# Kernel optimization log

Measured on AMD Instinct MI355X. Metric: run time of the kernel, lower is better.

The kernel has to match this reference:

```python
import jax, jax.numpy as jnp
import numpy as np

B, TQ, TP, H, A = 64, 64, 1024, 1024, 1024
NEG_INF = -1e30


def setup_inputs() -> dict:
    key = jax.random.key(0)
    ks = jax.random.split(key, 12)
    w = lambda k, shape, scale=0.02: (jax.random.normal(k, shape, jnp.float32) * scale)
    return dict(
        question=jax.random.normal(ks[0], (B, TQ, H), jnp.float32),
        question_mask=jnp.ones((B, TQ), jnp.float32),
        passage=jax.random.normal(ks[1], (B, TP, H), jnp.float32),
        passage_mask=jnp.ones((B, TP), jnp.float32),
        V_q=jax.random.normal(ks[2], (1, 1, H), jnp.float32),  # nn.Parameter(torch.randn)
        Wk_q=w(ks[3], (H, A)), Wq_q=w(ks[4], (H, A)), w_q=w(ks[5], (A,)),
        Wk_p=w(ks[6], (H, A)), Wq_p=w(ks[7], (H, A)), w_p=w(ks[8], (A,)),
        W_ih=w(ks[9], (3 * H, H)), W_hh=w(ks[10], (3 * H, H)),
        b_ih=jnp.zeros((3 * H,), jnp.float32), b_hh=jnp.zeros((3 * H,), jnp.float32),
    )


def _attn_pool(key_seq, query, mask, Wk, Wq, wv):
    """Additive attention pooling. key_seq: [T,B,H]; query: [1,B,Hq] or [1,1,Hq]
    (broadcasts over T and/or B); mask: [T,B]. Returns pooled [1,B,H], masked logits [T,B]."""
    s = jnp.tanh(key_seq @ Wk + query @ Wq) @ wv          # [T,B]
    s = jnp.where(mask > 0, s, NEG_INF)                    # mask invalid positions
    alpha = jax.nn.softmax(s, axis=0)                      # softmax over time
    pooled = jnp.einsum('tb,tbh->bh', alpha, key_seq)[None]
    return pooled, s


def _gru_cell(x, h, W_ih, W_hh, b_ih, b_hh):
    """torch.nn.GRUCell math. x, h: [B,H]."""
    gi = x @ W_ih.T + b_ih
    gh = h @ W_hh.T + b_hh
    i_r, i_z, i_n = jnp.split(gi, 3, axis=-1)
    h_r, h_z, h_n = jnp.split(gh, 3, axis=-1)
    r = jax.nn.sigmoid(i_r + h_r)
    z = jax.nn.sigmoid(i_z + h_z)
    n = jnp.tanh(i_n + r * h_n)
    return (1.0 - z) * n + z * h


def reference(question, question_mask, passage, passage_mask, V_q, Wk_q, Wq_q, w_q,
              Wk_p, Wq_p, w_p, W_ih, W_hh, b_ih, b_hh):
    # batch_first -> time-first
    q = jnp.transpose(question, (1, 0, 2))   # [TQ,B,H]
    qm = question_mask.T                     # [TQ,B]
    p = jnp.transpose(passage, (1, 0, 2))    # [TP,B,H]
    pm = passage_mask.T                      # [TP,B]
    # question pooling with learned query V_q (broadcast over T and B)
    hidden, _ = _attn_pool(q, V_q, qm, Wk_q, Wq_q, w_q)          # [1,B,H]
    # passage pooling with question summary as query -> start logits
    inputs, ans_begin = _attn_pool(p, hidden, pm, Wk_p, Wq_p, w_p)
    # one GRU decoding step (num_layers=1, no dropout/residual)
    out = _gru_cell(inputs[0], hidden[0], W_ih, W_hh, b_ih, b_hh)  # [B,H]
    # passage pooling with updated state -> end logits
    _, ans_end = _attn_pool(p, out[None], pm, Wk_p, Wq_p, w_p)
    return ans_begin.T, ans_end.T            # each [B,TP]
```

## Files before the change

kernel.cpp:

```cpp
#include <hip/hip_runtime.h>
#include <cstdint>
#include <cstddef>

typedef unsigned short u16;
typedef __bf16 bf16x8 __attribute__((ext_vector_type(8)));
typedef float floatx4 __attribute__((ext_vector_type(4)));

__device__ __forceinline__ u16 f32_to_bf16(float f) {
    unsigned u = __builtin_bit_cast(unsigned, f);
    u += 0x7fffu + ((u >> 16) & 1u);
    return (u16)(u >> 16);
}
__device__ __forceinline__ unsigned pack_bf16x2(float lo, float hi) {
    return (unsigned)f32_to_bf16(lo) | ((unsigned)f32_to_bf16(hi) << 16);
}
__device__ __forceinline__ float bf16_lo(unsigned u) {
    return __builtin_bit_cast(float, u << 16);
}
__device__ __forceinline__ float bf16_hi(unsigned u) {
    return __builtin_bit_cast(float, u & 0xffff0000u);
}
__device__ __forceinline__ float fast_tanh(float x) {
    float e = __expf(2.0f * x);
    return 1.0f - 2.0f * __builtin_amdgcn_rcpf(e + 1.0f);
}
__device__ __forceinline__ float fast_sigmoid(float x) {
    return __builtin_amdgcn_rcpf(1.0f + __expf(-x));
}
__device__ __forceinline__ void async_copy16(void* lds, const void* g) {
    __builtin_amdgcn_global_load_lds((const __attribute__((address_space(1))) void*)g,
                                     (__attribute__((address_space(3))) void*)lds,
                                     16, 0, 0);
}

__global__ __launch_bounds__(256) void conv_bf16_kernel(
    const float* __restrict__ in, u16* __restrict__ out)
{
    const size_t i = ((size_t)blockIdx.x * 256 + threadIdx.x) * 8;
    float4 a = *(const float4*)(in + i);
    float4 b = *(const float4*)(in + i + 4);
    uint4 o;
    o.x = pack_bf16x2(a.x, a.y);
    o.y = pack_bf16x2(a.z, a.w);
    o.z = pack_bf16x2(b.x, b.y);
    o.w = pack_bf16x2(b.z, b.w);
    *(uint4*)(out + i) = o;
}

__global__ __launch_bounds__(256) void transpose_bf16_kernel(
    const float* __restrict__ W, u16* __restrict__ WT, int K, int N)
{
    __shared__ float tile[32][33];
    const int k0 = blockIdx.y * 32, n0 = blockIdx.x * 32;
    const int tid = threadIdx.x;
#pragma unroll
    for (int i = 0; i < 4; ++i) {
        int e = tid + i * 256, rr = e >> 5, cc = e & 31;
        tile[rr][cc] = W[(size_t)(k0 + rr) * N + (n0 + cc)];
    }
    __syncthreads();
#pragma unroll
    for (int i = 0; i < 4; ++i) {
        int e = tid + i * 256, rr = e >> 5, cc = e & 31;
        WT[(size_t)(n0 + rr) * K + (k0 + cc)] = f32_to_bf16(tile[cc][rr]);
    }
}

__global__ __launch_bounds__(256) void vq_proj_kernel(
    const float* __restrict__ Vq, const float* __restrict__ Wq, float* __restrict__ out)
{
    const int a = blockIdx.x * 256 + threadIdx.x;
    const int h0 = blockIdx.y * 128;
    float acc = 0.f;
#pragma unroll 8
    for (int h = h0; h < h0 + 128; ++h)
        acc += Vq[h] * Wq[(size_t)h * 1024 + a];
    atomicAdd(&out[a], acc);
}

__global__ __launch_bounds__(256) void gemm_bf16_kernel(
    const u16* __restrict__ A, const u16* __restrict__ BT,
    u16* __restrict__ C, int M, int K, int N)
{
    __shared__ __align__(16) u16 As[128 * 32];
    __shared__ __align__(16) u16 Bs[128 * 32];
    const int tid  = threadIdx.x;
    const int lane = tid & 63;
    const int wave = tid >> 6;
    const int wm = (wave >> 1) * 64, wn = (wave & 1) * 64;
    const int quad = lane >> 4, lr = lane & 15;
    const int m0 = blockIdx.y * 128;
    const int n0 = blockIdx.x * 128;

    const int r0 = tid >> 2, c0 = (tid & 3) * 8;
    const u16* gA = A  + (size_t)(m0 + r0) * K + c0;
    const u16* gB = BT + (size_t)(n0 + r0) * K + c0;
    u16* lA0 = As + wave * 512;  u16* lA1 = lA0 + 2048;
    u16* lB0 = Bs + wave * 512;  u16* lB1 = lB0 + 2048;
    const size_t rowStride = (size_t)64 * K;

    floatx4 acc[4][4] = {};

    for (int k0 = 0; k0 < K; k0 += 32) {
        async_copy16(lA0, gA + k0);
        async_copy16(lA1, gA + rowStride + k0);
        async_copy16(lB0, gB + k0);
        async_copy16(lB1, gB + rowStride + k0);
        __syncthreads();
        bf16x8 af[4], bfr[4];
#pragma unroll
        for (int i = 0; i < 4; ++i)
            af[i] = *(const bf16x8*)(As + (wm + i * 16 + lr) * 32 + quad * 8);
#pragma unroll
        for (int j = 0; j < 4; ++j)
            bfr[j] = *(const bf16x8*)(Bs + (wn + j * 16 + lr) * 32 + quad * 8);
#pragma unroll
        for (int i = 0; i < 4; ++i)
#pragma unroll
            for (int j = 0; j < 4; ++j)
                acc[i][j] = __builtin_amdgcn_mfma_f32_16x16x32_bf16(af[i], bfr[j], acc[i][j], 0, 0, 0);
        __syncthreads();
    }
#pragma unroll
    for (int i = 0; i < 4; ++i) {
        int rb = m0 + wm + i * 16 + quad * 4;
#pragma unroll
        for (int j = 0; j < 4; ++j) {
            int col = n0 + wn + j * 16 + lr;
#pragma unroll
            for (int rg = 0; rg < 4; ++rg)
                C[(size_t)(rb + rg) * N + col] = f32_to_bf16(acc[i][j][rg]);
        }
    }
}

__global__ __launch_bounds__(256) void tanh_dot_kernel(
    const u16* __restrict__ R, const float* __restrict__ shift,
    const float* __restrict__ wv, const float* __restrict__ mask,
    float* __restrict__ out, int shiftDiv)
{
    const int row  = blockIdx.x * 4 + (threadIdx.x >> 6);
    const int lane = threadIdx.x & 63;
    const u16* rp   = R + (size_t)row * 1024;
    const float* sp = shift + (size_t)(row / shiftDiv) * 1024;
    float acc = 0.f;
#pragma unroll
    for (int p = 0; p < 2; ++p) {
        const int a0 = (p * 64 + lane) * 8;
        uint4  rv = *(const uint4*)(rp + a0);
        float4 s0 = *(const float4*)(sp + a0);
        float4 s1 = *(const float4*)(sp + a0 + 4);
        float4 w0 = *(const float4*)(wv + a0);
        float4 w1 = *(const float4*)(wv + a0 + 4);
        acc += fast_tanh(bf16_lo(rv.x) + s0.x) * w0.x;
        acc += fast_tanh(bf16_hi(rv.x) + s0.y) * w0.y;
        acc += fast_tanh(bf16_lo(rv.y) + s0.z) * w0.z;
        acc += fast_tanh(bf16_hi(rv.y) + s0.w) * w0.w;
        acc += fast_tanh(bf16_lo(rv.z) + s1.x) * w1.x;
        acc += fast_tanh(bf16_hi(rv.z) + s1.y) * w1.y;
        acc += fast_tanh(bf16_lo(rv.w) + s1.z) * w1.z;
        acc += fast_tanh(bf16_hi(rv.w) + s1.w) * w1.w;
    }
#pragma unroll
    for (int off = 32; off > 0; off >>= 1)
        acc += __shfl_down(acc, off, 64);
    if (lane == 0)
        out[row] = (mask[row] > 0.f) ? acc : -1e30f;
}

__global__ __launch_bounds__(256) void pool_q_kernel(
    const float* __restrict__ s, const float* __restrict__ seq, float* __restrict__ hidden)
{
    const int b = blockIdx.x, tid = threadIdx.x;
    __shared__ float alpha[64];
    if (tid < 64) {
        float v = s[b * 64 + tid];
        float m = v;
#pragma unroll
        for (int off = 32; off > 0; off >>= 1) m = fmaxf(m, __shfl_xor(m, off, 64));
        float e = __expf(v - m);
        float sum = e;
#pragma unroll
        for (int off = 32; off > 0; off >>= 1) sum += __shfl_xor(sum, off, 64);
        alpha[tid] = e * __builtin_amdgcn_rcpf(sum);
    }
    __syncthreads();
    float acc[4] = {0.f, 0.f, 0.f, 0.f};
    const float* base = seq + (size_t)b * 64 * 1024;
#pragma unroll 4
    for (int t = 0; t < 64; ++t) {
        const float a = alpha[t];
#pragma unroll
        for (int j = 0; j < 4; ++j)
            acc[j] += a * base[(size_t)t * 1024 + tid + j * 256];
    }
#pragma unroll
    for (int j = 0; j < 4; ++j) hidden[b * 1024 + tid + j * 256] = acc[j];
}

__global__ __launch_bounds__(256) void pool_p_kernel(
    const float* __restrict__ s, const float* __restrict__ seq, float* __restrict__ pooled)
{
    const int b = blockIdx.x, tid = threadIdx.x;
    const int col = blockIdx.y * 256 + tid;
    const int lane = tid & 63, wid = tid >> 6;
    __shared__ float alpha[1024];
    __shared__ float redm[4], reds[4];
    const float* sr = s + b * 1024;
    float v[4];
    float m = -3.4e38f;
#pragma unroll
    for (int j = 0; j < 4; ++j) { v[j] = sr[tid + j * 256]; m = fmaxf(m, v[j]); }
#pragma unroll
    for (int off = 32; off > 0; off >>= 1) m = fmaxf(m, __shfl_xor(m, off, 64));
    if (lane == 0) redm[wid] = m;
    __syncthreads();
    m = fmaxf(fmaxf(redm[0], redm[1]), fmaxf(redm[2], redm[3]));
    float sum = 0.f;
#pragma unroll
    for (int j = 0; j < 4; ++j) { float e = __expf(v[j] - m); alpha[tid + j * 256] = e; sum += e; }
#pragma unroll
    for (int off = 32; off > 0; off >>= 1) sum += __shfl_xor(sum, off, 64);
    if (lane == 0) reds[wid] = sum;
    __syncthreads();
    const float rs = __builtin_amdgcn_rcpf(reds[0] + reds[1] + reds[2] + reds[3]);
    float acc = 0.f;
    const float* base = seq + (size_t)b * (1024 * 1024) + col;
#pragma unroll 8
    for (int t = 0; t < 1024; ++t)
        acc += alpha[t] * base[(size_t)t * 1024];
    pooled[b * 1024 + col] = acc * rs;
}

template <bool BT, bool SPLIT>
__global__ __launch_bounds__(256) void small_gemm_kernel(
    const float* __restrict__ X0, const float* __restrict__ X1,
    const float* __restrict__ B0, const float* __restrict__ B1,
    float* __restrict__ out0, float* __restrict__ out1, int K, int N)
{
    const float* X  = blockIdx.y ? X1 : X0;
    const float* Bm = blockIdx.y ? B1 : B0;
    float* out      = blockIdx.y ? out1 : out0;
    const int n0 = blockIdx.x * 64;
    const int kBeg = SPLIT ? (int)blockIdx.z * (K >> 2) : 0;
    const int kEnd = SPLIT ? kBeg + (K >> 2) : K;
    const int tid = threadIdx.x, tx = tid & 15, ty = tid >> 4;
    __shared__ float Xs[64][17];
    __shared__ float Bs[64][17];
    float acc[4][4] = {};
    for (int kc = kBeg; kc < kEnd; kc += 16) {
        {
            int e = tid * 4, row = e >> 4, kk = e & 15;
            float4 v = *(const float4*)(X + (size_t)row * K + kc + kk);
            Xs[row][kk] = v.x; Xs[row][kk + 1] = v.y; Xs[row][kk + 2] = v.z; Xs[row][kk + 3] = v.w;
        }
        if (BT) {
            int e = tid * 4, n = e >> 4, kk = e & 15;
            float4 v = *(const float4*)(Bm + (size_t)(n0 + n) * K + kc + kk);
            Bs[n][kk] = v.x; Bs[n][kk + 1] = v.y; Bs[n][kk + 2] = v.z; Bs[n][kk + 3] = v.w;
        } else {
            int c = tid & 63, kb = tid >> 6;
#pragma unroll
            for (int u = 0; u < 4; ++u) {
                int k = kb + u * 4;
                Bs[c][k] = Bm[(size_t)(kc + k) * N + n0 + c];
            }
        }
        __syncthreads();
#pragma unroll
        for (int k = 0; k < 16; ++k) {
            float xr[4], br[4];
#pragma unroll
            for (int bi = 0; bi < 4; ++bi) xr[bi] = Xs[ty * 4 + bi][k];
#pragma unroll
            for (int ni = 0; ni < 4; ++ni) br[ni] = Bs[tx * 4 + ni][k];
#pragma unroll
            for (int bi = 0; bi < 4; ++bi)
#pragma unroll
                for (int ni = 0; ni < 4; ++ni)
                    acc[bi][ni] += xr[bi] * br[ni];
        }
        __syncthreads();
    }
#pragma unroll
    for (int bi = 0; bi < 4; ++bi)
#pragma unroll
        for (int ni = 0; ni < 4; ++ni) {
            float* p = out + (size_t)(ty * 4 + bi) * N + n0 + tx * 4 + ni;
            if (SPLIT) atomicAdd(p, acc[bi][ni]);
            else       *p = acc[bi][ni];
        }
}

__global__ __launch_bounds__(256) void gru_combine_kernel(
    const float* __restrict__ gi, const float* __restrict__ gh,
    const float* __restrict__ bih, const float* __restrict__ bhh,
    const float* __restrict__ h, float* __restrict__ out)
{
    const int idx = blockIdx.x * 256 + threadIdx.x;
    const int b = idx >> 10, j = idx & 1023;
    const float* gib = gi + (size_t)b * 3072;
    const float* ghb = gh + (size_t)b * 3072;
    float ir = gib[j] + bih[j],                hr = ghb[j] + bhh[j];
    float iz = gib[1024 + j] + bih[1024 + j],  hz = ghb[1024 + j] + bhh[1024 + j];
    float in_ = gib[2048 + j] + bih[2048 + j], hn = ghb[2048 + j] + bhh[2048 + j];
    float r = fast_sigmoid(ir + hr);
    float z = fast_sigmoid(iz + hz);
    float n = fast_tanh(in_ + r * hn);
    out[idx] = (1.f - z) * n + z * h[idx];
}

extern "C" void kernel_launch(void* const* d_in, const int* in_sizes, int n_in,
                              void* d_out, int out_size, void* d_ws, size_t ws_size,
                              hipStream_t stream)
{
    const float* question      = (const float*)d_in[0];
    const float* question_mask = (const float*)d_in[1];
    const float* passage       = (const float*)d_in[2];
    const float* passage_mask  = (const float*)d_in[3];
    const float* V_q  = (const float*)d_in[4];
    const float* Wk_q = (const float*)d_in[5];
    const float* Wq_q = (const float*)d_in[6];
    const float* w_q  = (const float*)d_in[7];
    const float* Wk_p = (const float*)d_in[8];
    const float* Wq_p = (const float*)d_in[9];
    const float* w_p  = (const float*)d_in[10];
    const float* W_ih = (const float*)d_in[11];
    const float* W_hh = (const float*)d_in[12];
    const float* b_ih = (const float*)d_in[13];
    const float* b_hh = (const float*)d_in[14];

    char* ws = (char*)d_ws;
    auto alloc = [&](size_t bytes) { char* p = ws; ws += (bytes + 255) & ~(size_t)255; return p; };
    u16* WkQT  = (u16*)alloc((size_t)1024 * 1024 * 2);
    u16* WkPT  = (u16*)alloc((size_t)1024 * 1024 * 2);
    u16* pbf   = (u16*)alloc((size_t)65536 * 1024 * 2);
    u16* qbf   = (u16*)alloc((size_t)4096 * 1024 * 2);
    u16* qWk   = (u16*)alloc((size_t)4096 * 1024 * 2);
    u16* pWk   = (u16*)alloc((size_t)65536 * 1024 * 2);
    float* vWq    = (float*)alloc(1024 * 4);
    float* s_q    = (float*)alloc(4096 * 4);
    float* hidden = (float*)alloc(65536 * 4);
    float* hWq    = (float*)alloc(65536 * 4);
    float* pooled = (float*)alloc(65536 * 4);
    float* gi     = (float*)alloc((size_t)64 * 3072 * 4);
    float* gh     = (float*)alloc((size_t)64 * 3072 * 4);
    float* gout   = (float*)alloc(65536 * 4);
    float* oWq    = (float*)alloc(65536 * 4);

    float* ans_begin = (float*)d_out;
    float* ans_end   = ans_begin + 65536;

    hipMemsetAsync(vWq, 0, 1024 * 4, stream);
    hipMemsetAsync(hWq, 0, 65536 * 4, stream);
    hipMemsetAsync(oWq, 0, 65536 * 4, stream);

    conv_bf16_kernel<<<dim3(32768), 256, 0, stream>>>(passage, pbf);
    conv_bf16_kernel<<<dim3(2048), 256, 0, stream>>>(question, qbf);
    transpose_bf16_kernel<<<dim3(32, 32), 256, 0, stream>>>(Wk_q, WkQT, 1024, 1024);
    transpose_bf16_kernel<<<dim3(32, 32), 256, 0, stream>>>(Wk_p, WkPT, 1024, 1024);

    gemm_bf16_kernel<<<dim3(8, 512), 256, 0, stream>>>(pbf, WkPT, pWk, 65536, 1024, 1024);

    gemm_bf16_kernel<<<dim3(8, 32), 256, 0, stream>>>(qbf, WkQT, qWk, 4096, 1024, 1024);
    vq_proj_kernel<<<dim3(4, 8), 256, 0, stream>>>(V_q, Wq_q, vWq);
    tanh_dot_kernel<<<dim3(1024), 256, 0, stream>>>(qWk, vWq, w_q, question_mask, s_q, 4096);
    pool_q_kernel<<<dim3(64), 256, 0, stream>>>(s_q, question, hidden);

    small_gemm_kernel<false, true><<<dim3(16, 1, 4), 256, 0, stream>>>(
        hidden, hidden, Wq_p, Wq_p, hWq, hWq, 1024, 1024);
    tanh_dot_kernel<<<dim3(16384), 256, 0, stream>>>(pWk, hWq, w_p, passage_mask, ans_begin, 1024);

    pool_p_kernel<<<dim3(64, 4), 256, 0, stream>>>(ans_begin, passage, pooled);
    small_gemm_kernel<true, false><<<dim3(48, 2), 256, 0, stream>>>(
        pooled, hidden, W_ih, W_hh, gi, gh, 1024, 3072);
    gru_combine_kernel<<<dim3(256), 256, 0, stream>>>(gi, gh, b_ih, b_hh, hidden, gout);

    small_gemm_kernel<false, true><<<dim3(16, 1, 4), 256, 0, stream>>>(
        gout, gout, Wq_p, Wq_p, oWq, oWq, 1024, 1024);
    tanh_dot_kernel<<<dim3(16384), 256, 0, stream>>>(pWk, oWq, w_p, passage_mask, ans_end, 1024);
}
```

Measured before the change: 990.8 us.

## Fuse begin-logit tanh-dot into passage GEMM epilogue and pool from bf16

The passage×Wk_p GEMM now adds the question-derived shift, applies tanh and dots with w_p in its epilogue, atomically accumulating the begin logits. This removes one full tanh_dot pass over the 128MB bf16 pWk tensor. Blocks are remapped with an XCD-aware swizzle. Passage pooling now reads the bf16 passage copy and is split over time into 4 chunks combined with atomics, halving its read traffic and adding parallelism at the cost of bf16 rounding and nondeterministic atomic sums. The GEMM still writes pWk because the end-logit pass needs it.

```diff
diff --git a/kernel.cpp b/kernel.cpp
--- a/kernel.cpp
+++ b/kernel.cpp
@@ -19,6 +19,9 @@
 }
 __device__ __forceinline__ float bf16_hi(unsigned u) {
     return __builtin_bit_cast(float, u & 0xffff0000u);
+}
+__device__ __forceinline__ float bf16f(u16 v) {
+    return __builtin_bit_cast(float, (unsigned)v << 16);
 }
 __device__ __forceinline__ float fast_tanh(float x) {
     float e = __expf(2.0f * x);
@@ -78,9 +81,11 @@
     atomicAdd(&out[a], acc);
 }
 
+template <bool FUSE>
 __global__ __launch_bounds__(256) void gemm_bf16_kernel(
     const u16* __restrict__ A, const u16* __restrict__ BT,
-    u16* __restrict__ C, int M, int K, int N)
+    u16* __restrict__ C, const float* __restrict__ shift,
+    const float* __restrict__ wv, float* __restrict__ sOut, int K, int N)
 {
     __shared__ __align__(16) u16 As[128 * 32];
     __shared__ __align__(16) u16 Bs[128 * 32];
@@ -89,8 +94,15 @@
     const int wave = tid >> 6;
     const int wm = (wave >> 1) * 64, wn = (wave & 1) * 64;
     const int quad = lane >> 4, lr = lane & 15;
-    const int m0 = blockIdx.y * 128;
-    const int n0 = blockIdx.x * 128;
+    int m0, n0;
+    if (FUSE) {
+        const int blk = blockIdx.x;
+        const int xcd = blk & 7, s = blk >> 3;
+        const int tx = s & 7, ty = ((s >> 3) << 3) | xcd;
+        m0 = ty * 128; n0 = tx * 128;
+    } else {
+        m0 = blockIdx.y * 128; n0 = blockIdx.x * 128;
+    }
 
     const int r0 = tid >> 2, c0 = (tid & 3) * 8;
     const u16* gA = A  + (size_t)(m0 + r0) * K + c0;
@@ -130,6 +142,31 @@
 #pragma unroll
             for (int rg = 0; rg < 4; ++rg)
                 C[(size_t)(rb + rg) * N + col] = f32_to_bf16(acc[i][j][rg]);
+        }
+    }
+    if (FUSE) {
+        const int b = m0 >> 10;
+        float hq[4], wp[4];
+#pragma unroll
+        for (int j = 0; j < 4; ++j) {
+            int col = n0 + wn + j * 16 + lr;
+            hq[j] = shift[b * 1024 + col];
+            wp[j] = wv[col];
+        }
+#pragma unroll
+        for (int i = 0; i < 4; ++i) {
+#pragma unroll
+            for (int rg = 0; rg < 4; ++rg) {
+                float t = 0.f;
+#pragma unroll
+                for (int j = 0; j < 4; ++j)
+                    t += fast_tanh(acc[i][j][rg] + hq[j]) * wp[j];
+#pragma unroll
+                for (int off = 1; off < 16; off <<= 1)
+                    t += __shfl_xor(t, off, 64);
+                if (lr == 0)
+                    atomicAdd(&sOut[m0 + wm + i * 16 + quad * 4 + rg], t);
+            }
         }
     }
 }
@@ -168,6 +205,13 @@
         out[row] = (mask[row] > 0.f) ? acc : -1e30f;
 }
 
+__global__ __launch_bounds__(256) void mask_kernel(
+    const float* __restrict__ sIn, const float* __restrict__ mask, float* __restrict__ out)
+{
+    const int idx = blockIdx.x * 256 + threadIdx.x;
+    out[idx] = (mask[idx] > 0.f) ? sIn[idx] : -1e30f;
+}
+
 __global__ __launch_bounds__(256) void pool_q_kernel(
     const float* __restrict__ s, const float* __restrict__ seq, float* __restrict__ hidden)
 {
@@ -199,10 +243,11 @@
 }
 
 __global__ __launch_bounds__(256) void pool_p_kernel(
-    const float* __restrict__ s, const float* __restrict__ seq, float* __restrict__ pooled)
+    const float* __restrict__ s, const u16* __restrict__ seq, float* __restrict__ pooled)
 {
     const int b = blockIdx.x, tid = threadIdx.x;
     const int col = blockIdx.y * 256 + tid;
+    const int t0 = blockIdx.z * 256;
     const int lane = tid & 63, wid = tid >> 6;
     __shared__ float alpha[1024];
     __shared__ float redm[4], reds[4];
@@ -225,11 +270,11 @@
     __syncthreads();
     const float rs = __builtin_amdgcn_rcpf(reds[0] + reds[1] + reds[2] + reds[3]);
     float acc = 0.f;
-    const float* base = seq + (size_t)b * (1024 * 1024) + col;
+    const u16* base = seq + (size_t)b * (1024 * 1024) + (size_t)t0 * 1024 + col;
 #pragma unroll 8
-    for (int t = 0; t < 1024; ++t)
-        acc += alpha[t] * base[(size_t)t * 1024];
-    pooled[b * 1024 + col] = acc * rs;
+    for (int t = 0; t < 256; ++t)
+        acc += alpha[t0 + t] * bf16f(base[(size_t)t * 1024]);
+    atomicAdd(&pooled[b * 1024 + col], acc * rs);
 }
 
 template <bool BT, bool SPLIT>
@@ -342,6 +387,7 @@
     float* s_q    = (float*)alloc(4096 * 4);
     float* hidden = (float*)alloc(65536 * 4);
     float* hWq    = (float*)alloc(65536 * 4);
+    float* sBegin = (float*)alloc(65536 * 4);
     float* pooled = (float*)alloc(65536 * 4);
     float* gi     = (float*)alloc((size_t)64 * 3072 * 4);
     float* gh     = (float*)alloc((size_t)64 * 3072 * 4);
@@ -354,24 +400,27 @@
     hipMemsetAsync(vWq, 0, 1024 * 4, stream);
     hipMemsetAsync(hWq, 0, 65536 * 4, stream);
     hipMemsetAsync(oWq, 0, 65536 * 4, stream);
+    hipMemsetAsync(sBegin, 0, 65536 * 4, stream);
+    hipMemsetAsync(pooled, 0, 65536 * 4, stream);
 
     conv_bf16_kernel<<<dim3(32768), 256, 0, stream>>>(passage, pbf);
     conv_bf16_kernel<<<dim3(2048), 256, 0, stream>>>(question, qbf);
     transpose_bf16_kernel<<<dim3(32, 32), 256, 0, stream>>>(Wk_q, WkQT, 1024, 1024);
     transpose_bf16_kernel<<<dim3(32, 32), 256, 0, stream>>>(Wk_p, WkPT, 1024, 1024);
 
-    gemm_bf16_kernel<<<dim3(8, 512), 256, 0, stream>>>(pbf, WkPT, pWk, 65536, 1024, 1024);
-
-    gemm_bf16_kernel<<<dim3(8, 32), 256, 0, stream>>>(qbf, WkQT, qWk, 4096, 1024, 1024);
+    gemm_bf16_kernel<false><<<dim3(8, 32), 256, 0, stream>>>(
+        qbf, WkQT, qWk, nullptr, nullptr, nullptr, 1024, 1024);
     vq_proj_kernel<<<dim3(4, 8), 256, 0, stream>>>(V_q, Wq_q, vWq);
     tanh_dot_kernel<<<dim3(1024), 256, 0, stream>>>(qWk, vWq, w_q, question_mask, s_q, 4096);
     pool_q_kernel<<<dim3(64), 256, 0, stream>>>(s_q, question, hidden);
-
     small_gemm_kernel<false, true><<<dim3(16, 1, 4), 256, 0, stream>>>(
         hidden, hidden, Wq_p, Wq_p, hWq, hWq, 1024, 1024);
-    tanh_dot_kernel<<<dim3(16384), 256, 0, stream>>>(pWk, hWq, w_p, passage_mask, ans_begin, 1024);
-
-    pool_p_kernel<<<dim3(64, 4), 256, 0, stream>>>(ans_begin, passage, pooled);
+
+    gemm_bf16_kernel<true><<<dim3(4096), 256, 0, stream>>>(
+        pbf, WkPT, pWk, hWq, w_p, sBegin, 1024, 1024);
+    mask_kernel<<<dim3(256), 256, 0, stream>>>(sBegin, passage_mask, ans_begin);
+
+    pool_p_kernel<<<dim3(64, 4, 4), 256, 0, stream>>>(ans_begin, pbf, pooled);
     small_gemm_kernel<true, false><<<dim3(48, 2), 256, 0, stream>>>(
         pooled, hidden, W_ih, W_hh, gi, gh, 1024, 3072);
     gru_combine_kernel<<<dim3(256), 256, 0, stream>>>(gi, gh, b_ih, b_hh, hidden, gout);
```

Result: faster. 911.5 us (-8.0%).
